# Kernel tuning notes

Measured on AMD Instinct MI355X. Metric: run time of the kernel, lower is better.

Reference implementation:

```python
import jax, jax.numpy as jnp
import numpy as np

NUM_HEADS = 1
HIDDEN = 256
HEAD_DIM = HIDDEN // NUM_HEADS
SCALE = HEAD_DIM ** -0.5


def _rotate_pairwise(x):
    # (... , d) -> rotate adjacent pairs: (x0,x1,x2,x3,..) -> (-x1,x0,-x3,x2,..)
    shape = x.shape
    x = x.reshape(*shape[:-1], -1, 2)
    x = jnp.stack([-x[..., 1], x[..., 0]], axis=-1)
    return x.reshape(shape)


def setup_inputs() -> dict:
    key = jax.random.key(0)
    ks = jax.random.split(key, 12)
    B, PB, QS, KS = 1, 1, 4096, 16448
    KV_IN = 64
    d = {
        'query': jax.random.normal(ks[0], (B, PB, QS, HIDDEN), jnp.float32),
        'key': jax.random.normal(ks[1], (B, PB, KS, KV_IN), jnp.float32),
        'value': jax.random.normal(ks[2], (B, PB, KS, KV_IN), jnp.float32),
        'rope_cos': jax.random.normal(ks[3], (QS, HEAD_DIM), jnp.float32),
        'rope_sin': jax.random.normal(ks[4], (QS, HEAD_DIM), jnp.float32),
        'wq': jax.random.normal(ks[5], (HIDDEN, HIDDEN), jnp.float32) * (HIDDEN ** -0.5),
        'bq': jnp.zeros((HIDDEN,), jnp.float32),
        'wk': jax.random.normal(ks[6], (KV_IN, HIDDEN), jnp.float32) * (KV_IN ** -0.5),
        'bk': jnp.zeros((HIDDEN,), jnp.float32),
        'wv': jax.random.normal(ks[7], (KV_IN, HIDDEN), jnp.float32) * (KV_IN ** -0.5),
        'bv': jnp.zeros((HIDDEN,), jnp.float32),
        'wo': jax.random.normal(ks[8], (HIDDEN, HIDDEN), jnp.float32) * (HIDDEN ** -0.5),
        'bo': jnp.zeros((HIDDEN,), jnp.float32),
        'num_k_exclude_rope': 64,
    }
    return d


def reference(query, key, value, rope_cos, rope_sin, wq, bq, wk, bk, wv, bv, wo, bo, num_k_exclude_rope):
    batch, pb, qs, _ = query.shape
    ks = key.shape[2]
    B = batch * pb
    # projections -> [B, H, S, hd]
    q = (query @ wq + bq).reshape(B, qs, NUM_HEADS, HEAD_DIM).transpose(0, 2, 1, 3)
    k = (key @ wk + bk).reshape(B, ks, NUM_HEADS, HEAD_DIM).transpose(0, 2, 1, 3)
    v = (value @ wv + bv).reshape(B, ks, NUM_HEADS, HEAD_DIM).transpose(0, 2, 1, 3)
    cos = rope_cos[None, None]  # [1,1,QS,hd]
    sin = rope_sin[None, None]
    # split off non-RoPE keys (object pointer tokens)
    n_rot = ks - num_k_exclude_rope
    k_rot, k_pass = k[:, :, :n_rot, :], k[:, :, n_rot:, :]
    q = q * cos + _rotate_pairwise(q) * sin
    if n_rot != qs:  # rope_k_repeat branch (static shapes)
        rep = n_rot // qs
        cos_k = jnp.repeat(cos, rep, axis=2)
        sin_k = jnp.repeat(sin, rep, axis=2)
    else:
        cos_k, sin_k = cos, sin
    k_emb = k_rot * cos_k + _rotate_pairwise(k_rot) * sin_k
    k = jnp.concatenate([k_emb, k_pass], axis=-2)
    attn = jax.nn.softmax(jnp.einsum('bhqd,bhkd->bhqk', q * SCALE, k), axis=-1)
    x = jnp.einsum('bhqk,bhkd->bhqd', attn, v)
    x = x.transpose(0, 2, 1, 3).reshape(batch, pb, qs, HIDDEN)
    return x @ wo + bo
```

## Files before the change

kernel.cpp:

```cpp
#include <hip/hip_runtime.h>
#include <hip/hip_bf16.h>

typedef __attribute__((ext_vector_type(4))) float floatx4;
typedef __attribute__((ext_vector_type(8))) short shortx8;
typedef __attribute__((ext_vector_type(8))) _Float16 halfx8;
typedef _Float16 half_t;

#define MFMA_BF16(A,B,C) __builtin_amdgcn_mfma_f32_16x16x32_bf16((A),(B),(C),0,0,0)
#define NEG_INF (-__builtin_inff())
#define GLOBAL_AS __attribute__((address_space(1)))
#define LDS_AS __attribute__((address_space(3)))

static __device__ __forceinline__ unsigned short f2b(float f) {
    union { float f; unsigned u; } v; v.f = f;
    unsigned r = v.u + 0x7FFFu + ((v.u >> 16) & 1u);
    return (unsigned short)(r >> 16);
}
static __device__ __forceinline__ unsigned pack_bf16(float lo, float hi) {
    return (unsigned)f2b(lo) | ((unsigned)f2b(hi) << 16);
}
static __device__ __forceinline__ unsigned pack_half(float lo, float hi) {
    union { half_t h[2]; unsigned u; } p;
    p.h[0] = (half_t)lo; p.h[1] = (half_t)hi;
    return p.u;
}
static __device__ __forceinline__ float EXP2F(float x) { return __builtin_amdgcn_exp2f(x); }

#define NSPLIT 8
#define NSPLIT_C 16
#define NTILES 257

__global__ __launch_bounds__(256) void wtrans_kernel(
    const float* __restrict__ wq, const float* __restrict__ wk,
    const float* __restrict__ wv, const float* __restrict__ wo,
    unsigned short* __restrict__ wqt, unsigned short* __restrict__ wkt,
    unsigned short* __restrict__ wvt, unsigned short* __restrict__ wot)
{
    __shared__ unsigned short tb[64 * 68];
    const int bid = blockIdx.x, tid = threadIdx.x;
    const float* src; unsigned short* dst; int K0, N0, Kfull;
    if (bid < 16)      { src = wq; dst = wqt; Kfull = 256; K0 = (bid >> 2) * 64; N0 = (bid & 3) * 64; }
    else if (bid < 20) { src = wk; dst = wkt; Kfull = 64;  K0 = 0; N0 = (bid - 16) * 64; }
    else if (bid < 24) { src = wv; dst = wvt; Kfull = 64;  K0 = 0; N0 = (bid - 20) * 64; }
    else { int t2 = bid - 24; src = wo; dst = wot; Kfull = 256; K0 = (t2 >> 2) * 64; N0 = (t2 & 3) * 64; }

    {
        const int r = tid >> 2, c0 = (tid & 3) * 16;
        const float* p = src + (K0 + r) * 256 + N0 + c0;
        #pragma unroll
        for (int j = 0; j < 16; j += 4) {
            floatx4 f = *(const floatx4*)(p + j);
            tb[r * 68 + c0 + j + 0] = f2b(f[0]);
            tb[r * 68 + c0 + j + 1] = f2b(f[1]);
            tb[r * 68 + c0 + j + 2] = f2b(f[2]);
            tb[r * 68 + c0 + j + 3] = f2b(f[3]);
        }
    }
    __syncthreads();
    {
        const int n = tid >> 2, k0 = (tid & 3) * 16;
        shortx8 v0, v1;
        #pragma unroll
        for (int j = 0; j < 8; j++) {
            v0[j] = tb[(k0 + j) * 68 + n];
            v1[j] = tb[(k0 + 8 + j) * 68 + n];
        }
        unsigned short* q = dst + (N0 + n) * Kfull + K0 + k0;
        *(shortx8*)q = v0;
        *(shortx8*)(q + 8) = v1;
    }
}

__global__ __launch_bounds__(256) void proj_kernel(
    const float* __restrict__ query, const float* __restrict__ key,
    const float* __restrict__ value,
    const unsigned short* __restrict__ wqt, const float* __restrict__ bq,
    const unsigned short* __restrict__ wkt, const float* __restrict__ bk,
    const unsigned short* __restrict__ wvt, const float* __restrict__ bv,
    const float* __restrict__ cosb, const float* __restrict__ sinb,
    const int* __restrict__ nkx,
    unsigned short* __restrict__ qr, unsigned short* __restrict__ krw,
    unsigned short* __restrict__ vtg)
{
    __shared__ unsigned short tbuf[256 * 72];
    const int tid = threadIdx.x;
    const int wave = tid >> 6, lane = tid & 63;
    const int c = lane & 15, quad = lane >> 4;
    const int bx = blockIdx.x;

    if (bx < 64) {
        const int m0 = bx * 64;
        shortx8 aA[8];
        {
            const int mrow = m0 + wave * 16 + c;
            #pragma unroll
            for (int ks = 0; ks < 8; ks++) {
                const float* p = query + mrow * 256 + ks * 32 + quad * 8;
                floatx4 f0 = *(const floatx4*)p;
                floatx4 f1 = *(const floatx4*)(p + 4);
                shortx8 a;
                #pragma unroll
                for (int j = 0; j < 4; j++) { a[j] = (short)f2b(f0[j]); a[j + 4] = (short)f2b(f1[j]); }
                aA[ks] = a;
            }
        }
        floatx4 acc[16];
        #pragma unroll
        for (int nt = 0; nt < 16; nt++) { acc[nt][0]=0.f; acc[nt][1]=0.f; acc[nt][2]=0.f; acc[nt][3]=0.f; }
        #pragma unroll
        for (int nt = 0; nt < 16; nt++) {
            #pragma unroll
            for (int ks = 0; ks < 8; ks++) {
                shortx8 b = *(const shortx8*)(wqt + (nt * 16 + c) * 256 + ks * 32 + quad * 8);
                acc[nt] = MFMA_BF16(aA[ks], b, acc[nt]);
            }
        }
        const float sc = 0.09016844005556021f;
        #pragma unroll
        for (int nt = 0; nt < 16; nt++) {
            const int col = nt * 16 + c;
            float vals[4];
            #pragma unroll
            for (int r = 0; r < 4; r++) {
                const int row = m0 + wave * 16 + quad * 4 + r;
                float v = acc[nt][r] + bq[col];
                float partner = __shfl_xor(v, 1);
                float cv = cosb[row * 256 + col];
                float sn = sinb[row * 256 + col];
                float rot = (col & 1) ? partner : -partner;
                vals[r] = (v * cv + rot * sn) * sc;
            }
            #pragma unroll
            for (int r2 = 0; r2 < 4; r2 += 2) {
                float a = vals[r2], b = vals[r2 + 1];
                float ax = __shfl_xor(a, 1), bx2 = __shfl_xor(b, 1);
                float lo = (c & 1) ? bx2 : a;
                float hi = (c & 1) ? b : ax;
                int row = m0 + wave * 16 + quad * 4 + r2 + (c & 1);
                *(unsigned*)(qr + row * 256 + nt * 16 + (c & ~1)) = pack_bf16(lo, hi);
            }
        }
        return;
    }

    const int isv = (bx >= 321);
    const int m0 = (isv ? (bx - 321) : (bx - 64)) * 64;
    const float* src = isv ? value : key;
    const unsigned short* wt = isv ? wvt : wkt;
    const float* bias = isv ? bv : bk;

    shortx8 aA[2];
    {
        const int mrow = m0 + wave * 16 + c;
        #pragma unroll
        for (int ks = 0; ks < 2; ks++) {
            const float* p = src + mrow * 64 + ks * 32 + quad * 8;
            floatx4 f0 = *(const floatx4*)p;
            floatx4 f1 = *(const floatx4*)(p + 4);
            shortx8 a;
            #pragma unroll
            for (int j = 0; j < 4; j++) { a[j] = (short)f2b(f0[j]); a[j + 4] = (short)f2b(f1[j]); }
            aA[ks] = a;
        }
    }
    floatx4 acc[16];
    #pragma unroll
    for (int nt = 0; nt < 16; nt++) { acc[nt][0]=0.f; acc[nt][1]=0.f; acc[nt][2]=0.f; acc[nt][3]=0.f; }
    #pragma unroll
    for (int nt = 0; nt < 16; nt++) {
        #pragma unroll
        for (int ks = 0; ks < 2; ks++) {
            shortx8 b = *(const shortx8*)(wt + (nt * 16 + c) * 64 + ks * 32 + quad * 8);
            acc[nt] = MFMA_BF16(aA[ks], b, acc[nt]);
        }
    }
    if (!isv) {
        const int n_rot = 16448 - nkx[0];
        int rep = n_rot / 4096; if (rep < 1) rep = 1;
        int rc4[4];
        #pragma unroll
        for (int r = 0; r < 4; r++) {
            int row = m0 + wave * 16 + quad * 4 + r;
            rc4[r] = row / rep;
        }
        #pragma unroll
        for (int nt = 0; nt < 16; nt++) {
            const int col = nt * 16 + c;
            float vals[4];
            #pragma unroll
            for (int r = 0; r < 4; r++) {
                const int row = m0 + wave * 16 + quad * 4 + r;
                float v = acc[nt][r] + bias[col];
                float partner = __shfl_xor(v, 1);
                float outv = v;
                if (row < n_rot) {
                    float cv = cosb[rc4[r] * 256 + col];
                    float sn = sinb[rc4[r] * 256 + col];
                    float rot = (col & 1) ? partner : -partner;
                    outv = v * cv + rot * sn;
                }
                vals[r] = outv;
            }
            #pragma unroll
            for (int r2 = 0; r2 < 4; r2 += 2) {
                float a = vals[r2], b = vals[r2 + 1];
                float ax = __shfl_xor(a, 1), bx2 = __shfl_xor(b, 1);
                float lo = (c & 1) ? bx2 : a;
                float hi = (c & 1) ? b : ax;
                int row = m0 + wave * 16 + quad * 4 + r2 + (c & 1);
                *(unsigned*)(krw + row * 256 + nt * 16 + (c & ~1)) = pack_bf16(lo, hi);
            }
        }
    } else {
        #pragma unroll
        for (int nt = 0; nt < 16; nt++) {
            const int col = nt * 16 + c;
            #pragma unroll
            for (int r = 0; r < 4; r++) {
                const int rl = wave * 16 + quad * 4 + r;
                tbuf[col * 72 + rl] = f2b(acc[nt][r] + bias[col]);
            }
        }
        __syncthreads();
        #pragma unroll
        for (int i = 0; i < 8; i++) {
            int G = i * 256 + tid;
            int n = G >> 3, g = G & 7;
            *(floatx4*)(vtg + n * 16448 + m0 + g * 8) = *(const floatx4*)(tbuf + n * 72 + g * 8);
        }
    }
}

__global__ __launch_bounds__(512, 2) void flash_kernel(
    const unsigned short* __restrict__ qr, const unsigned short* __restrict__ kr,
    const unsigned short* __restrict__ vt, half_t* __restrict__ Opart,
    float* __restrict__ Lpart)
{
    __shared__ unsigned short smem[75776];
    const int tid = threadIdx.x;
    const int wave = tid >> 6, lane = tid & 63;
    const int c = lane & 15, quad = lane >> 4;
    const int cx = c & 7;
    const int qg = wave & 3, kvh = wave >> 2;
    const int qrow0 = blockIdx.x * 128 + qg * 32;
    const int s = blockIdx.y;
    const int t0 = (s * NTILES) / NSPLIT, t1 = ((s + 1) * NTILES) / NSPLIT;
    unsigned short* pw = smem + 65536 + wave * 1280;

    shortx8 aQ[2][8];
    #pragma unroll
    for (int u = 0; u < 2; u++)
        #pragma unroll
        for (int ks = 0; ks < 8; ks++)
            aQ[u][ks] = *(const shortx8*)(qr + (qrow0 + u * 16 + c) * 256 + ks * 32 + quad * 8);

    floatx4 o[2][16];
    #pragma unroll
    for (int u = 0; u < 2; u++)
        #pragma unroll
        for (int nt = 0; nt < 16; nt++) { o[u][nt][0]=0.f; o[u][nt][1]=0.f; o[u][nt][2]=0.f; o[u][nt][3]=0.f; }
    float l_i[2] = { 0.f, 0.f };

    auto stage = [&](int t, int buf) {
        const int kv0 = t * 64;
        unsigned short* kb = smem + buf * 16384;
        unsigned short* vb = smem + 32768 + buf * 16384;
        #pragma unroll
        for (int i = 0; i < 4; i++) {
            int L = i * 512 + tid;
            int kv = L >> 5, p = L & 31;
            int g = (p & 24) | ((p & 7) ^ (kv & 7));
            __builtin_amdgcn_global_load_lds(
                (const GLOBAL_AS void*)(const void*)(kr + (kv0 + kv) * 256 + g * 8),
                (LDS_AS void*)(void*)(kb + (i * 512 + wave * 64) * 8), 16, 0, 0);
        }
        #pragma unroll
        for (int i = 0; i < 4; i++) {
            int L = i * 512 + tid;
            int d = L >> 3, p = L & 7;
            int g = p ^ (d & 7);
            __builtin_amdgcn_global_load_lds(
                (const GLOBAL_AS void*)(const void*)(vt + d * 16448 + kv0 + g * 8),
                (LDS_AS void*)(void*)(vb + (i * 512 + wave * 64) * 8), 16, 0, 0);
        }
    };

    stage(t0, 0);
    int cur = 0;
    const int pv_p = (kvh * 4 + quad) ^ cx;
    for (int t = t0; t < t1; t++) {
        __syncthreads();
        if (t + 1 < t1) stage(t + 1, cur ^ 1);
        const unsigned short* kb = smem + cur * 16384;
        const unsigned short* vb = smem + 32768 + cur * 16384;

        floatx4 sv[2][2];
        #pragma unroll
        for (int u = 0; u < 2; u++)
            #pragma unroll
            for (int nt = 0; nt < 2; nt++) { sv[u][nt][0]=0.f; sv[u][nt][1]=0.f; sv[u][nt][2]=0.f; sv[u][nt][3]=0.f; }
        #pragma unroll
        for (int nt = 0; nt < 2; nt++) {
            const unsigned short* krow = kb + (kvh * 32 + nt * 16 + c) * 256;
            #pragma unroll
            for (int ks = 0; ks < 8; ks++) {
                int p = ((ks >> 1) * 8) | ((((ks & 1) << 2) + quad) ^ cx);
                shortx8 kfrag = *(const shortx8*)(krow + p * 8);
                sv[0][nt] = MFMA_BF16(kfrag, aQ[0][ks], sv[0][nt]);
                sv[1][nt] = MFMA_BF16(kfrag, aQ[1][ks], sv[1][nt]);
            }
        }
        #pragma unroll
        for (int u = 0; u < 2; u++) {
            float rs = 0.f;
            #pragma unroll
            for (int nt = 0; nt < 2; nt++)
                #pragma unroll
                for (int r = 0; r < 4; r++) {
                    float pv = EXP2F(sv[u][nt][r]);
                    sv[u][nt][r] = pv;
                    rs += pv;
                }
            l_i[u] += rs;
        }
        #pragma unroll
        for (int u = 0; u < 2; u++)
            #pragma unroll
            for (int nt = 0; nt < 2; nt++)
                #pragma unroll
                for (int r2 = 0; r2 < 4; r2 += 2)
                    *(unsigned*)(pw + (u * 16 + c) * 40 + nt * 16 + quad * 4 + r2) =
                        pack_bf16(sv[u][nt][r2], sv[u][nt][r2 + 1]);
        shortx8 aP[2];
        #pragma unroll
        for (int u = 0; u < 2; u++)
            aP[u] = *(const shortx8*)(pw + (u * 16 + c) * 40 + quad * 8);
        #pragma unroll
        for (int nt = 0; nt < 16; nt++) {
            const unsigned short* vrow = vb + (nt * 16 + c) * 64;
            shortx8 b0 = *(const shortx8*)(vrow + pv_p * 8);
            o[0][nt] = MFMA_BF16(aP[0], b0, o[0][nt]);
            o[1][nt] = MFMA_BF16(aP[1], b0, o[1][nt]);
        }
        cur ^= 1;
    }
    const int sEff = s * 2 + kvh;
    half_t* Ob = Opart + (size_t)sEff * (4096 * 256);
    #pragma unroll
    for (int u = 0; u < 2; u++) {
        l_i[u] += __shfl_xor(l_i[u], 16);
        l_i[u] += __shfl_xor(l_i[u], 32);
    }
    float inv[2] = { 1.0f / l_i[0], 1.0f / l_i[1] };
    #pragma unroll
    for (int u = 0; u < 2; u++) {
        float ar[4];
        #pragma unroll
        for (int r = 0; r < 4; r++) ar[r] = __shfl(inv[u], quad * 4 + r);
        #pragma unroll
        for (int nt = 0; nt < 16; nt++) {
            o[u][nt][0] *= ar[0]; o[u][nt][1] *= ar[1];
            o[u][nt][2] *= ar[2]; o[u][nt][3] *= ar[3];
        }
    }
    #pragma unroll
    for (int u = 0; u < 2; u++)
        #pragma unroll
        for (int nt = 0; nt < 16; nt++)
            #pragma unroll
            for (int r2 = 0; r2 < 4; r2 += 2) {
                float a = o[u][nt][r2], b = o[u][nt][r2 + 1];
                float ax = __shfl_xor(a, 1), bx2 = __shfl_xor(b, 1);
                float lo = (c & 1) ? bx2 : a;
                float hi = (c & 1) ? b : ax;
                int row = qrow0 + u * 16 + quad * 4 + r2 + (c & 1);
                *(unsigned*)(Ob + row * 256 + nt * 16 + (c & ~1)) = pack_half(lo, hi);
            }
    if (quad == 0) {
        #pragma unroll
        for (int u = 0; u < 2; u++)
            Lpart[sEff * 4096 + qrow0 + u * 16 + c] = l_i[u];
    }
}

__global__ __launch_bounds__(256) void combine_kernel(
    const half_t* __restrict__ Opart, const float* __restrict__ Lpart,
    unsigned short* __restrict__ xb)
{
    int idx = blockIdx.x * 256 + threadIdx.x;
    int row = idx >> 5;
    int d0 = (idx & 31) * 8;
    float wn[NSPLIT_C], den = 0.f;
    #pragma unroll
    for (int sp = 0; sp < NSPLIT_C; sp++) { wn[sp] = Lpart[sp * 4096 + row]; den += wn[sp]; }
    float inv = 1.0f / den;
    #pragma unroll
    for (int sp = 0; sp < NSPLIT_C; sp++) wn[sp] *= inv;
    float acc[8];
    #pragma unroll
    for (int j = 0; j < 8; j++) acc[j] = 0.f;
    #pragma unroll
    for (int sp = 0; sp < NSPLIT_C; sp++) {
        halfx8 hv = *(const halfx8*)(Opart + (size_t)sp * (4096 * 256) + row * 256 + d0);
        #pragma unroll
        for (int j = 0; j < 8; j++) acc[j] += wn[sp] * (float)hv[j];
    }
    shortx8 xv;
    #pragma unroll
    for (int j = 0; j < 8; j++) xv[j] = (short)f2b(acc[j]);
    *(shortx8*)(xb + row * 256 + d0) = xv;
}

__global__ __launch_bounds__(256) void oproj_kernel(
    const unsigned short* __restrict__ xb, const unsigned short* __restrict__ wot,
    const float* __restrict__ bo, float* __restrict__ outp)
{
    const int tid = threadIdx.x;
    const int wave = tid >> 6, lane = tid & 63;
    const int c = lane & 15, quad = lane >> 4;
    const int m0 = blockIdx.x * 64;
    const int n0 = blockIdx.y * 64;

    shortx8 aX[8];
    #pragma unroll
    for (int ks = 0; ks < 8; ks++)
        aX[ks] = *(const shortx8*)(xb + (m0 + wave * 16 + c) * 256 + ks * 32 + quad * 8);
    floatx4 acc[4];
    #pragma unroll
    for (int nt = 0; nt < 4; nt++) { acc[nt][0]=0.f; acc[nt][1]=0.f; acc[nt][2]=0.f; acc[nt][3]=0.f; }
    #pragma unroll
    for (int nt = 0; nt < 4; nt++) {
        #pragma unroll
        for (int ks = 0; ks < 8; ks++) {
            shortx8 b = *(const shortx8*)(wot + (n0 + nt * 16 + c) * 256 + ks * 32 + quad * 8);
            acc[nt] = MFMA_BF16(aX[ks], b, acc[nt]);
        }
    }
    #pragma unroll
    for (int nt = 0; nt < 4; nt++) {
        const int col = n0 + nt * 16 + c;
        #pragma unroll
        for (int r = 0; r < 4; r++) {
            const int row = m0 + wave * 16 + quad * 4 + r;
            outp[row * 256 + col] = acc[nt][r] + bo[col];
        }
    }
}

extern "C" void kernel_launch(void* const* d_in, const int* in_sizes, int n_in,
                              void* d_out, int out_size, void* d_ws, size_t ws_size,
                              hipStream_t stream) {
    const float* query = (const float*)d_in[0];
    const float* key   = (const float*)d_in[1];
    const float* value = (const float*)d_in[2];
    const float* cosb  = (const float*)d_in[3];
    const float* sinb  = (const float*)d_in[4];
    const float* wq    = (const float*)d_in[5];
    const float* bq    = (const float*)d_in[6];
    const float* wk    = (const float*)d_in[7];
    const float* bk    = (const float*)d_in[8];
    const float* wv    = (const float*)d_in[9];
    const float* bv    = (const float*)d_in[10];
    const float* wo    = (const float*)d_in[11];
    const float* bo    = (const float*)d_in[12];
    const int*   nk    = (const int*)d_in[13];

    char* ws = (char*)d_ws;
    unsigned short* wqt = (unsigned short*)(ws + 0);
    unsigned short* wkt = (unsigned short*)(ws + 131072);
    unsigned short* wvt = (unsigned short*)(ws + 163840);
    unsigned short* wot = (unsigned short*)(ws + 196608);
    unsigned short* qr  = (unsigned short*)(ws + 327680);
    unsigned short* xb  = (unsigned short*)(ws + 327680);
    unsigned short* krw = (unsigned short*)(ws + 2424832);
    unsigned short* vtg = (unsigned short*)(ws + 10846208);
    half_t* Opart = (half_t*)(ws + 19267584);
    float* Lpart = (float*)(ws + 52822016);
    float* outp  = (float*)d_out;

    wtrans_kernel<<<dim3(40), dim3(256), 0, stream>>>(wq, wk, wv, wo, wqt, wkt, wvt, wot);
    proj_kernel<<<dim3(578), dim3(256), 0, stream>>>(
        query, key, value, wqt, bq, wkt, bk, wvt, bv, cosb, sinb, nk, qr, krw, vtg);
    flash_kernel<<<dim3(32, NSPLIT), dim3(512), 0, stream>>>(qr, krw, vtg, Opart, Lpart);
    combine_kernel<<<dim3(512), dim3(256), 0, stream>>>(Opart, Lpart, xb);
    oproj_kernel<<<dim3(64, 4), dim3(256), 0, stream>>>(xb, wot, bo, outp);
}
```

Before: 230.7 us.

## Fuse all five stages into one cooperative persistent kernel with grid syncs

Replaces the five separate launches (weight transpose, projections, flash attention, combine, output projection) with one cooperative kernel of 256 blocks that moves between stages using grid-wide syncs. Work that used to be spread over many blocks is remapped onto the persistent grid, with two virtual blocks per 512-thread block and multiple passes. The combine and output projection appear to be merged so the intermediate x buffer is staged in shared memory rather than global memory. This removes launch gaps and some global round trips, at the cost of grid-sync overhead, a fixed grid size, and possibly lower occupancy or load imbalance in the projection stages.

```diff
diff --git a/kernel.cpp b/kernel.cpp
--- a/kernel.cpp
+++ b/kernel.cpp
@@ -1,5 +1,8 @@
 #include <hip/hip_runtime.h>
 #include <hip/hip_bf16.h>
+#include <hip/hip_cooperative_groups.h>
+
+namespace cg = cooperative_groups;
 
 typedef __attribute__((ext_vector_type(4))) float floatx4;
 typedef __attribute__((ext_vector_type(8))) short shortx8;
@@ -7,7 +10,6 @@
 typedef _Float16 half_t;
 
 #define MFMA_BF16(A,B,C) __builtin_amdgcn_mfma_f32_16x16x32_bf16((A),(B),(C),0,0,0)
-#define NEG_INF (-__builtin_inff())
 #define GLOBAL_AS __attribute__((address_space(1)))
 #define LDS_AS __attribute__((address_space(3)))
 
@@ -30,419 +32,422 @@
 #define NSPLIT_C 16
 #define NTILES 257
 
-__global__ __launch_bounds__(256) void wtrans_kernel(
-    const float* __restrict__ wq, const float* __restrict__ wk,
-    const float* __restrict__ wv, const float* __restrict__ wo,
+__global__ __launch_bounds__(512, 2) void mega_kernel(
+    const float* __restrict__ query, const float* __restrict__ key,
+    const float* __restrict__ value, const float* __restrict__ cosb,
+    const float* __restrict__ sinb,
+    const float* __restrict__ wq, const float* __restrict__ bq,
+    const float* __restrict__ wk, const float* __restrict__ bk,
+    const float* __restrict__ wv, const float* __restrict__ bv,
+    const float* __restrict__ wo, const float* __restrict__ bo,
+    const int* __restrict__ nkx,
     unsigned short* __restrict__ wqt, unsigned short* __restrict__ wkt,
-    unsigned short* __restrict__ wvt, unsigned short* __restrict__ wot)
+    unsigned short* __restrict__ wvt, unsigned short* __restrict__ wot,
+    unsigned short* __restrict__ qr, unsigned short* __restrict__ krw,
+    unsigned short* __restrict__ vtg, half_t* __restrict__ Opart,
+    float* __restrict__ Lpart, float* __restrict__ outp)
 {
-    __shared__ unsigned short tb[64 * 68];
-    const int bid = blockIdx.x, tid = threadIdx.x;
-    const float* src; unsigned short* dst; int K0, N0, Kfull;
-    if (bid < 16)      { src = wq; dst = wqt; Kfull = 256; K0 = (bid >> 2) * 64; N0 = (bid & 3) * 64; }
-    else if (bid < 20) { src = wk; dst = wkt; Kfull = 64;  K0 = 0; N0 = (bid - 16) * 64; }
-    else if (bid < 24) { src = wv; dst = wvt; Kfull = 64;  K0 = 0; N0 = (bid - 20) * 64; }
-    else { int t2 = bid - 24; src = wo; dst = wot; Kfull = 256; K0 = (t2 >> 2) * 64; N0 = (t2 & 3) * 64; }
-
-    {
-        const int r = tid >> 2, c0 = (tid & 3) * 16;
-        const float* p = src + (K0 + r) * 256 + N0 + c0;
-        #pragma unroll
-        for (int j = 0; j < 16; j += 4) {
-            floatx4 f = *(const floatx4*)(p + j);
-            tb[r * 68 + c0 + j + 0] = f2b(f[0]);
-            tb[r * 68 + c0 + j + 1] = f2b(f[1]);
-            tb[r * 68 + c0 + j + 2] = f2b(f[2]);
-            tb[r * 68 + c0 + j + 3] = f2b(f[3]);
-        }
-    }
-    __syncthreads();
-    {
-        const int n = tid >> 2, k0 = (tid & 3) * 16;
-        shortx8 v0, v1;
-        #pragma unroll
-        for (int j = 0; j < 8; j++) {
-            v0[j] = tb[(k0 + j) * 68 + n];
-            v1[j] = tb[(k0 + 8 + j) * 68 + n];
-        }
-        unsigned short* q = dst + (N0 + n) * Kfull + K0 + k0;
-        *(shortx8*)q = v0;
-        *(shortx8*)(q + 8) = v1;
-    }
-}
-
-__global__ __launch_bounds__(256) void proj_kernel(
-    const float* __restrict__ query, const float* __restrict__ key,
-    const float* __restrict__ value,
-    const unsigned short* __restrict__ wqt, const float* __restrict__ bq,
-    const unsigned short* __restrict__ wkt, const float* __restrict__ bk,
-    const unsigned short* __restrict__ wvt, const float* __restrict__ bv,
-    const float* __restrict__ cosb, const float* __restrict__ sinb,
-    const int* __restrict__ nkx,
-    unsigned short* __restrict__ qr, unsigned short* __restrict__ krw,
-    unsigned short* __restrict__ vtg)
-{
-    __shared__ unsigned short tbuf[256 * 72];
-    const int tid = threadIdx.x;
-    const int wave = tid >> 6, lane = tid & 63;
-    const int c = lane & 15, quad = lane >> 4;
-    const int bx = blockIdx.x;
-
-    if (bx < 64) {
-        const int m0 = bx * 64;
-        shortx8 aA[8];
-        {
-            const int mrow = m0 + wave * 16 + c;
-            #pragma unroll
-            for (int ks = 0; ks < 8; ks++) {
-                const float* p = query + mrow * 256 + ks * 32 + quad * 8;
-                floatx4 f0 = *(const floatx4*)p;
-                floatx4 f1 = *(const floatx4*)(p + 4);
-                shortx8 a;
-                #pragma unroll
-                for (int j = 0; j < 4; j++) { a[j] = (short)f2b(f0[j]); a[j + 4] = (short)f2b(f1[j]); }
-                aA[ks] = a;
-            }
-        }
-        floatx4 acc[16];
-        #pragma unroll
-        for (int nt = 0; nt < 16; nt++) { acc[nt][0]=0.f; acc[nt][1]=0.f; acc[nt][2]=0.f; acc[nt][3]=0.f; }
-        #pragma unroll
-        for (int nt = 0; nt < 16; nt++) {
-            #pragma unroll
-            for (int ks = 0; ks < 8; ks++) {
-                shortx8 b = *(const shortx8*)(wqt + (nt * 16 + c) * 256 + ks * 32 + quad * 8);
-                acc[nt] = MFMA_BF16(aA[ks], b, acc[nt]);
-            }
-        }
-        const float sc = 0.09016844005556021f;
-        #pragma unroll
-        for (int nt = 0; nt < 16; nt++) {
-            const int col = nt * 16 + c;
-            float vals[4];
-            #pragma unroll
-            for (int r = 0; r < 4; r++) {
-                const int row = m0 + wave * 16 + quad * 4 + r;
-                float v = acc[nt][r] + bq[col];
-                float partner = __shfl_xor(v, 1);
-                float cv = cosb[row * 256 + col];
-                float sn = sinb[row * 256 + col];
-                float rot = (col & 1) ? partner : -partner;
-                vals[r] = (v * cv + rot * sn) * sc;
-            }
-            #pragma unroll
-            for (int r2 = 0; r2 < 4; r2 += 2) {
-                float a = vals[r2], b = vals[r2 + 1];
-                float ax = __shfl_xor(a, 1), bx2 = __shfl_xor(b, 1);
-                float lo = (c & 1) ? bx2 : a;
-                float hi = (c & 1) ? b : ax;
-                int row = m0 + wave * 16 + quad * 4 + r2 + (c & 1);
-                *(unsigned*)(qr + row * 256 + nt * 16 + (c & ~1)) = pack_bf16(lo, hi);
-            }
-        }
-        return;
-    }
-
-    const int isv = (bx >= 321);
-    const int m0 = (isv ? (bx - 321) : (bx - 64)) * 64;
-    const float* src = isv ? value : key;
-    const unsigned short* wt = isv ? wvt : wkt;
-    const float* bias = isv ? bv : bk;
-
-    shortx8 aA[2];
-    {
-        const int mrow = m0 + wave * 16 + c;
-        #pragma unroll
-        for (int ks = 0; ks < 2; ks++) {
-            const float* p = src + mrow * 64 + ks * 32 + quad * 8;
-            floatx4 f0 = *(const floatx4*)p;
-            floatx4 f1 = *(const floatx4*)(p + 4);
-            shortx8 a;
-            #pragma unroll
-            for (int j = 0; j < 4; j++) { a[j] = (short)f2b(f0[j]); a[j + 4] = (short)f2b(f1[j]); }
-            aA[ks] = a;
-        }
-    }
-    floatx4 acc[16];
-    #pragma unroll
-    for (int nt = 0; nt < 16; nt++) { acc[nt][0]=0.f; acc[nt][1]=0.f; acc[nt][2]=0.f; acc[nt][3]=0.f; }
-    #pragma unroll
-    for (int nt = 0; nt < 16; nt++) {
-        #pragma unroll
-        for (int ks = 0; ks < 2; ks++) {
-            shortx8 b = *(const shortx8*)(wt + (nt * 16 + c) * 64 + ks * 32 + quad * 8);
-            acc[nt] = MFMA_BF16(aA[ks], b, acc[nt]);
-        }
-    }
-    if (!isv) {
-        const int n_rot = 16448 - nkx[0];
-        int rep = n_rot / 4096; if (rep < 1) rep = 1;
-        int rc4[4];
-        #pragma unroll
-        for (int r = 0; r < 4; r++) {
-            int row = m0 + wave * 16 + quad * 4 + r;
-            rc4[r] = row / rep;
-        }
-        #pragma unroll
-        for (int nt = 0; nt < 16; nt++) {
-            const int col = nt * 16 + c;
-            float vals[4];
-            #pragma unroll
-            for (int r = 0; r < 4; r++) {
-                const int row = m0 + wave * 16 + quad * 4 + r;
-                float v = acc[nt][r] + bias[col];
-                float partner = __shfl_xor(v, 1);
-                float outv = v;
-                if (row < n_rot) {
-                    float cv = cosb[rc4[r] * 256 + col];
-                    float sn = sinb[rc4[r] * 256 + col];
-                    float rot = (col & 1) ? partner : -partner;
-                    outv = v * cv + rot * sn;
-                }
-                vals[r] = outv;
-            }
-            #pragma unroll
-            for (int r2 = 0; r2 < 4; r2 += 2) {
-                float a = vals[r2], b = vals[r2 + 1];
-                float ax = __shfl_xor(a, 1), bx2 = __shfl_xor(b, 1);
-                float lo = (c & 1) ? bx2 : a;
-                float hi = (c & 1) ? b : ax;
-                int row = m0 + wave * 16 + quad * 4 + r2 + (c & 1);
-                *(unsigned*)(krw + row * 256 + nt * 16 + (c & ~1)) = pack_bf16(lo, hi);
-            }
-        }
-    } else {
-        #pragma unroll
-        for (int nt = 0; nt < 16; nt++) {
-            const int col = nt * 16 + c;
-            #pragma unroll
-            for (int r = 0; r < 4; r++) {
-                const int rl = wave * 16 + quad * 4 + r;
-                tbuf[col * 72 + rl] = f2b(acc[nt][r] + bias[col]);
-            }
-        }
-        __syncthreads();
-        #pragma unroll
-        for (int i = 0; i < 8; i++) {
-            int G = i * 256 + tid;
-            int n = G >> 3, g = G & 7;
-            *(floatx4*)(vtg + n * 16448 + m0 + g * 8) = *(const floatx4*)(tbuf + n * 72 + g * 8);
-        }
-    }
-}
-
-__global__ __launch_bounds__(512, 2) void flash_kernel(
-    const unsigned short* __restrict__ qr, const unsigned short* __restrict__ kr,
-    const unsigned short* __restrict__ vt, half_t* __restrict__ Opart,
-    float* __restrict__ Lpart)
-{
+    cg::grid_group grid = cg::this_grid();
     __shared__ unsigned short smem[75776];
     const int tid = threadIdx.x;
-    const int wave = tid >> 6, lane = tid & 63;
-    const int c = lane & 15, quad = lane >> 4;
-    const int cx = c & 7;
-    const int qg = wave & 3, kvh = wave >> 2;
-    const int qrow0 = blockIdx.x * 128 + qg * 32;
-    const int s = blockIdx.y;
-    const int t0 = (s * NTILES) / NSPLIT, t1 = ((s + 1) * NTILES) / NSPLIT;
-    unsigned short* pw = smem + 65536 + wave * 1280;
-
-    shortx8 aQ[2][8];
-    #pragma unroll
-    for (int u = 0; u < 2; u++)
+    const int bid = blockIdx.x;
+
+    if (bid < 20) {
+        const int sub = tid >> 8, t = tid & 255;
+        const int vb = bid * 2 + sub;
+        unsigned short* tb = smem + sub * 4608;
+        const float* srcw; unsigned short* dstw; int K0, N0, Kfull;
+        if (vb < 16)      { srcw = wq; dstw = wqt; Kfull = 256; K0 = (vb >> 2) * 64; N0 = (vb & 3) * 64; }
+        else if (vb < 20) { srcw = wk; dstw = wkt; Kfull = 64;  K0 = 0; N0 = (vb - 16) * 64; }
+        else if (vb < 24) { srcw = wv; dstw = wvt; Kfull = 64;  K0 = 0; N0 = (vb - 20) * 64; }
+        else { int t2 = vb - 24; srcw = wo; dstw = wot; Kfull = 256; K0 = (t2 >> 2) * 64; N0 = (t2 & 3) * 64; }
+        {
+            const int r = t >> 2, c0 = (t & 3) * 16;
+            const float* p = srcw + (K0 + r) * 256 + N0 + c0;
+            #pragma unroll
+            for (int j = 0; j < 16; j += 4) {
+                floatx4 f = *(const floatx4*)(p + j);
+                tb[r * 68 + c0 + j + 0] = f2b(f[0]);
+                tb[r * 68 + c0 + j + 1] = f2b(f[1]);
+                tb[r * 68 + c0 + j + 2] = f2b(f[2]);
+                tb[r * 68 + c0 + j + 3] = f2b(f[3]);
+            }
+        }
+        __syncthreads();
+        {
+            const int n = t >> 2, k0 = (t & 3) * 16;
+            shortx8 v0, v1;
+            #pragma unroll
+            for (int j = 0; j < 8; j++) {
+                v0[j] = tb[(k0 + j) * 68 + n];
+                v1[j] = tb[(k0 + 8 + j) * 68 + n];
+            }
+            unsigned short* q = dstw + (N0 + n) * Kfull + K0 + k0;
+            *(shortx8*)q = v0;
+            *(shortx8*)(q + 8) = v1;
+        }
+    }
+    grid.sync();
+
+    #pragma unroll 1
+    for (int pass = 0; pass < 2; pass++) {
+        const int sub = tid >> 8, t = tid & 255;
+        const int vb = pass * 512 + bid * 2 + sub;
+        const int wave = t >> 6, lane = t & 63;
+        const int c = lane & 15, quad = lane >> 4;
+        unsigned short* tbuf = smem + sub * 18432;
+        int vM0 = 0;
+        bool doV = false;
+
+        if (vb < 64) {
+            const int m0 = vb * 64;
+            shortx8 aA[8];
+            {
+                const int mrow = m0 + wave * 16 + c;
+                #pragma unroll
+                for (int ks = 0; ks < 8; ks++) {
+                    const float* p = query + mrow * 256 + ks * 32 + quad * 8;
+                    floatx4 f0 = *(const floatx4*)p;
+                    floatx4 f1 = *(const floatx4*)(p + 4);
+                    shortx8 a;
+                    #pragma unroll
+                    for (int j = 0; j < 4; j++) { a[j] = (short)f2b(f0[j]); a[j + 4] = (short)f2b(f1[j]); }
+                    aA[ks] = a;
+                }
+            }
+            floatx4 acc[16];
+            #pragma unroll
+            for (int nt = 0; nt < 16; nt++) { acc[nt][0]=0.f; acc[nt][1]=0.f; acc[nt][2]=0.f; acc[nt][3]=0.f; }
+            #pragma unroll
+            for (int nt = 0; nt < 16; nt++) {
+                #pragma unroll
+                for (int ks = 0; ks < 8; ks++) {
+                    shortx8 b = *(const shortx8*)(wqt + (nt * 16 + c) * 256 + ks * 32 + quad * 8);
+                    acc[nt] = MFMA_BF16(aA[ks], b, acc[nt]);
+                }
+            }
+            const float sc = 0.09016844005556021f;
+            #pragma unroll
+            for (int nt = 0; nt < 16; nt++) {
+                const int col = nt * 16 + c;
+                float vals[4];
+                #pragma unroll
+                for (int r = 0; r < 4; r++) {
+                    const int row = m0 + wave * 16 + quad * 4 + r;
+                    float v = acc[nt][r] + bq[col];
+                    float partner = __shfl_xor(v, 1);
+                    float cv = cosb[row * 256 + col];
+                    float sn = sinb[row * 256 + col];
+                    float rot = (col & 1) ? partner : -partner;
+                    vals[r] = (v * cv + rot * sn) * sc;
+                }
+                #pragma unroll
+                for (int r2 = 0; r2 < 4; r2 += 2) {
+                    float a = vals[r2], b = vals[r2 + 1];
+                    float ax = __shfl_xor(a, 1), bx2 = __shfl_xor(b, 1);
+                    float lo = (c & 1) ? bx2 : a;
+                    float hi = (c & 1) ? b : ax;
+                    int row = m0 + wave * 16 + quad * 4 + r2 + (c & 1);
+                    *(unsigned*)(qr + row * 256 + nt * 16 + (c & ~1)) = pack_bf16(lo, hi);
+                }
+            }
+        } else if (vb < 578) {
+            const int isv = (vb >= 321);
+            const int m0 = (isv ? (vb - 321) : (vb - 64)) * 64;
+            const float* src = isv ? value : key;
+            const unsigned short* wt = isv ? wvt : wkt;
+            const float* bias = isv ? bv : bk;
+
+            shortx8 aA[2];
+            {
+                const int mrow = m0 + wave * 16 + c;
+                #pragma unroll
+                for (int ks = 0; ks < 2; ks++) {
+                    const float* p = src + mrow * 64 + ks * 32 + quad * 8;
+                    floatx4 f0 = *(const floatx4*)p;
+                    floatx4 f1 = *(const floatx4*)(p + 4);
+                    shortx8 a;
+                    #pragma unroll
+                    for (int j = 0; j < 4; j++) { a[j] = (short)f2b(f0[j]); a[j + 4] = (short)f2b(f1[j]); }
+                    aA[ks] = a;
+                }
+            }
+            floatx4 acc[16];
+            #pragma unroll
+            for (int nt = 0; nt < 16; nt++) { acc[nt][0]=0.f; acc[nt][1]=0.f; acc[nt][2]=0.f; acc[nt][3]=0.f; }
+            #pragma unroll
+            for (int nt = 0; nt < 16; nt++) {
+                #pragma unroll
+                for (int ks = 0; ks < 2; ks++) {
+                    shortx8 b = *(const shortx8*)(wt + (nt * 16 + c) * 64 + ks * 32 + quad * 8);
+                    acc[nt] = MFMA_BF16(aA[ks], b, acc[nt]);
+                }
+            }
+            if (!isv) {
+                const int n_rot = 16448 - nkx[0];
+                int rep = n_rot / 4096; if (rep < 1) rep = 1;
+                int rc4[4];
+                #pragma unroll
+                for (int r = 0; r < 4; r++) {
+                    int row = m0 + wave * 16 + quad * 4 + r;
+                    rc4[r] = row / rep;
+                }
+                #pragma unroll
+                for (int nt = 0; nt < 16; nt++) {
+                    const int col = nt * 16 + c;
+                    float vals[4];
+                    #pragma unroll
+                    for (int r = 0; r < 4; r++) {
+                        const int row = m0 + wave * 16 + quad * 4 + r;
+                        float v = acc[nt][r] + bias[col];
+                        float partner = __shfl_xor(v, 1);
+                        float outv = v;
+                        if (row < n_rot) {
+                            float cv = cosb[rc4[r] * 256 + col];
+                            float sn = sinb[rc4[r] * 256 + col];
+                            float rot = (col & 1) ? partner : -partner;
+                            outv = v * cv + rot * sn;
+                        }
+                        vals[r] = outv;
+                    }
+                    #pragma unroll
+                    for (int r2 = 0; r2 < 4; r2 += 2) {
+                        float a = vals[r2], b = vals[r2 + 1];
+                        float ax = __shfl_xor(a, 1), bx2 = __shfl_xor(b, 1);
+                        float lo = (c & 1) ? bx2 : a;
+                        float hi = (c & 1) ? b : ax;
+                        int row = m0 + wave * 16 + quad * 4 + r2 + (c & 1);
+                        *(unsigned*)(krw + row * 256 + nt * 16 + (c & ~1)) = pack_bf16(lo, hi);
+                    }
+                }
+            } else {
+                #pragma unroll
+                for (int nt = 0; nt < 16; nt++) {
+                    const int col = nt * 16 + c;
+                    #pragma unroll
+                    for (int r = 0; r < 4; r++) {
+                        const int rl = wave * 16 + quad * 4 + r;
+                        tbuf[col * 72 + rl] = f2b(acc[nt][r] + bias[col]);
+                    }
+                }
+                doV = true;
+                vM0 = m0;
+            }
+        }
+        __syncthreads();
+        if (doV) {
+            #pragma unroll
+            for (int i = 0; i < 8; i++) {
+                int G = i * 256 + t;
+                int n = G >> 3, g = G & 7;
+                *(floatx4*)(vtg + n * 16448 + vM0 + g * 8) = *(const floatx4*)(tbuf + n * 72 + g * 8);
+            }
+        }
+        __syncthreads();
+    }
+    grid.sync();
+
+    {
+        const int wave = tid >> 6, lane = tid & 63;
+        const int c = lane & 15, quad = lane >> 4;
+        const int cx = c & 7;
+        const int qg = wave & 3, kvh = wave >> 2;
+        const int qrow0 = (bid & 31) * 128 + qg * 32;
+        const int s = bid >> 5;
+        const int t0 = (s * NTILES) / NSPLIT, t1 = ((s + 1) * NTILES) / NSPLIT;
+        unsigned short* pw = smem + 65536 + wave * 1280;
+
+        shortx8 aQ[2][8];
+        #pragma unroll
+        for (int u = 0; u < 2; u++)
+            #pragma unroll
+            for (int ks = 0; ks < 8; ks++)
+                aQ[u][ks] = *(const shortx8*)(qr + (qrow0 + u * 16 + c) * 256 + ks * 32 + quad * 8);
+
+        floatx4 o[2][16];
+        #pragma unroll
+        for (int u = 0; u < 2; u++)
+            #pragma unroll
+            for (int nt = 0; nt < 16; nt++) { o[u][nt][0]=0.f; o[u][nt][1]=0.f; o[u][nt][2]=0.f; o[u][nt][3]=0.f; }
+        float l_i[2] = { 0.f, 0.f };
+
+        auto stage = [&](int t, int buf) {
+            const int kv0 = t * 64;
+            unsigned short* kb = smem + buf * 16384;
+            unsigned short* vb = smem + 32768 + buf * 16384;
+            #pragma unroll
+            for (int i = 0; i < 4; i++) {
+                int L = i * 512 + tid;
+                int kv = L >> 5, p = L & 31;
+                int g = (p & 24) | ((p & 7) ^ (kv & 7));
+                __builtin_amdgcn_global_load_lds(
+                    (const GLOBAL_AS void*)(const void*)(krw + (kv0 + kv) * 256 + g * 8),
+                    (LDS_AS void*)(void*)(kb + (i * 512 + wave * 64) * 8), 16, 0, 0);
+            }
+            #pragma unroll
+            for (int i = 0; i < 4; i++) {
+                int L = i * 512 + tid;
+                int d = L >> 3, p = L & 7;
+                int g = p ^ (d & 7);
+                __builtin_amdgcn_global_load_lds(
+                    (const GLOBAL_AS void*)(const void*)(vtg + d * 16448 + kv0 + g * 8),
+                    (LDS_AS void*)(void*)(vb + (i * 512 + wave * 64) * 8), 16, 0, 0);
+            }
+        };
+
+        stage(t0, 0);
+        int cur = 0;
+        const int pv_p = (kvh * 4 + quad) ^ cx;
+        for (int t = t0; t < t1; t++) {
+            __syncthreads();
+            if (t + 1 < t1) stage(t + 1, cur ^ 1);
+            const unsigned short* kb = smem + cur * 16384;
+            const unsigned short* vb = smem + 32768 + cur * 16384;
+
+            floatx4 sv[2][2];
+            #pragma unroll
+            for (int u = 0; u < 2; u++)
+                #pragma unroll
+                for (int nt = 0; nt < 2; nt++) { sv[u][nt][0]=0.f; sv[u][nt][1]=0.f; sv[u][nt][2]=0.f; sv[u][nt][3]=0.f; }
+            #pragma unroll
+            for (int nt = 0; nt < 2; nt++) {
+                const unsigned short* krow = kb + (kvh * 32 + nt * 16 + c) * 256;
+                #pragma unroll
+                for (int ks = 0; ks < 8; ks++) {
+                    int p = ((ks >> 1) * 8) | ((((ks & 1) << 2) + quad) ^ cx);
+                    shortx8 kfrag = *(const shortx8*)(krow + p * 8);
+                    sv[0][nt] = MFMA_BF16(kfrag, aQ[0][ks], sv[0][nt]);
+                    sv[1][nt] = MFMA_BF16(kfrag, aQ[1][ks], sv[1][nt]);
+                }
+            }
+            #pragma unroll
+            for (int u = 0; u < 2; u++) {
+                float rs = 0.f;
+                #pragma unroll
+                for (int nt = 0; nt < 2; nt++)
+                    #pragma unroll
+                    for (int r = 0; r < 4; r++) {
+                        float pv = EXP2F(sv[u][nt][r]);
+                        sv[u][nt][r] = pv;
+                        rs += pv;
+                    }
+                l_i[u] += rs;
+            }
+            #pragma unroll
+            for (int u = 0; u < 2; u++)
+                #pragma unroll
+                for (int nt = 0; nt < 2; nt++)
+                    #pragma unroll
+                    for (int r2 = 0; r2 < 4; r2 += 2)
+                        *(unsigned*)(pw + (u * 16 + c) * 40 + nt * 16 + quad * 4 + r2) =
+                            pack_bf16(sv[u][nt][r2], sv[u][nt][r2 + 1]);
+            shortx8 aP[2];
+            #pragma unroll
+            for (int u = 0; u < 2; u++)
+                aP[u] = *(const shortx8*)(pw + (u * 16 + c) * 40 + quad * 8);
+            #pragma unroll
+            for (int nt = 0; nt < 16; nt++) {
+                const unsigned short* vrow = vb + (nt * 16 + c) * 64;
+                shortx8 b0 = *(const shortx8*)(vrow + pv_p * 8);
+                o[0][nt] = MFMA_BF16(aP[0], b0, o[0][nt]);
+                o[1][nt] = MFMA_BF16(aP[1], b0, o[1][nt]);
+            }
+            cur ^= 1;
+        }
+        const int sEff = s * 2 + kvh;
+        half_t* Ob = Opart + (size_t)sEff * (4096 * 256);
+        #pragma unroll
+        for (int u = 0; u < 2; u++) {
+            l_i[u] += __shfl_xor(l_i[u], 16);
+            l_i[u] += __shfl_xor(l_i[u], 32);
+        }
+        float inv[2] = { 1.0f / l_i[0], 1.0f / l_i[1] };
+        #pragma unroll
+        for (int u = 0; u < 2; u++) {
+            float ar[4];
+            #pragma unroll
+            for (int r = 0; r < 4; r++) ar[r] = __shfl(inv[u], quad * 4 + r);
+            #pragma unroll
+            for (int nt = 0; nt < 16; nt++) {
+                o[u][nt][0] *= ar[0]; o[u][nt][1] *= ar[1];
+                o[u][nt][2] *= ar[2]; o[u][nt][3] *= ar[3];
+            }
+        }
+        #pragma unroll
+        for (int u = 0; u < 2; u++)
+            #pragma unroll
+            for (int nt = 0; nt < 16; nt++)
+                #pragma unroll
+                for (int r2 = 0; r2 < 4; r2 += 2) {
+                    float a = o[u][nt][r2], b = o[u][nt][r2 + 1];
+                    float ax = __shfl_xor(a, 1), bx2 = __shfl_xor(b, 1);
+                    float lo = (c & 1) ? bx2 : a;
+                    float hi = (c & 1) ? b : ax;
+                    int row = qrow0 + u * 16 + quad * 4 + r2 + (c & 1);
+                    *(unsigned*)(Ob + row * 256 + nt * 16 + (c & ~1)) = pack_half(lo, hi);
+                }
+        if (quad == 0) {
+            #pragma unroll
+            for (int u = 0; u < 2; u++)
+                Lpart[sEff * 4096 + qrow0 + u * 16 + c] = l_i[u];
+        }
+    }
+    grid.sync();
+
+    {
+        const int m0 = bid * 16;
+        unsigned short* xb = smem;
+        {
+            const int r_l = tid >> 5;
+            const int d0 = (tid & 31) * 8;
+            const int row = m0 + r_l;
+            float wn[NSPLIT_C], den = 0.f;
+            #pragma unroll
+            for (int sp = 0; sp < NSPLIT_C; sp++) { wn[sp] = Lpart[sp * 4096 + row]; den += wn[sp]; }
+            float inv = 1.0f / den;
+            #pragma unroll
+            for (int sp = 0; sp < NSPLIT_C; sp++) wn[sp] *= inv;
+            float acc[8];
+            #pragma unroll
+            for (int j = 0; j < 8; j++) acc[j] = 0.f;
+            #pragma unroll
+            for (int sp = 0; sp < NSPLIT_C; sp++) {
+                halfx8 hv = *(const halfx8*)(Opart + (size_t)sp * (4096 * 256) + row * 256 + d0);
+                #pragma unroll
+                for (int j = 0; j < 8; j++) acc[j] += wn[sp] * (float)hv[j];
+            }
+            shortx8 xv;
+            #pragma unroll
+            for (int j = 0; j < 8; j++) xv[j] = (short)f2b(acc[j]);
+            *(shortx8*)(xb + r_l * 264 + d0) = xv;
+        }
+        __syncthreads();
+        const int wave = tid >> 6, lane = tid & 63;
+        const int c = lane & 15, quad = lane >> 4;
+        shortx8 aX[8];
         #pragma unroll
         for (int ks = 0; ks < 8; ks++)
-            aQ[u][ks] = *(const shortx8*)(qr + (qrow0 + u * 16 + c) * 256 + ks * 32 + quad * 8);
-
-    floatx4 o[2][16];
-    #pragma unroll
-    for (int u = 0; u < 2; u++)
-        #pragma unroll
-        for (int nt = 0; nt < 16; nt++) { o[u][nt][0]=0.f; o[u][nt][1]=0.f; o[u][nt][2]=0.f; o[u][nt][3]=0.f; }
-    float l_i[2] = { 0.f, 0.f };
-
-    auto stage = [&](int t, int buf) {
-        const int kv0 = t * 64;
-        unsigned short* kb = smem + buf * 16384;
-        unsigned short* vb = smem + 32768 + buf * 16384;
-        #pragma unroll
-        for (int i = 0; i < 4; i++) {
-            int L = i * 512 + tid;
-            int kv = L >> 5, p = L & 31;
-            int g = (p & 24) | ((p & 7) ^ (kv & 7));
-            __builtin_amdgcn_global_load_lds(
-                (const GLOBAL_AS void*)(const void*)(kr + (kv0 + kv) * 256 + g * 8),
-                (LDS_AS void*)(void*)(kb + (i * 512 + wave * 64) * 8), 16, 0, 0);
-        }
-        #pragma unroll
-        for (int i = 0; i < 4; i++) {
-            int L = i * 512 + tid;
-            int d = L >> 3, p = L & 7;
-            int g = p ^ (d & 7);
-            __builtin_amdgcn_global_load_lds(
-                (const GLOBAL_AS void*)(const void*)(vt + d * 16448 + kv0 + g * 8),
-                (LDS_AS void*)(void*)(vb + (i * 512 + wave * 64) * 8), 16, 0, 0);
-        }
-    };
-
-    stage(t0, 0);
-    int cur = 0;
-    const int pv_p = (kvh * 4 + quad) ^ cx;
-    for (int t = t0; t < t1; t++) {
-        __syncthreads();
-        if (t + 1 < t1) stage(t + 1, cur ^ 1);
-        const unsigned short* kb = smem + cur * 16384;
-        const unsigned short* vb = smem + 32768 + cur * 16384;
-
-        floatx4 sv[2][2];
-        #pragma unroll
-        for (int u = 0; u < 2; u++)
-            #pragma unroll
-            for (int nt = 0; nt < 2; nt++) { sv[u][nt][0]=0.f; sv[u][nt][1]=0.f; sv[u][nt][2]=0.f; sv[u][nt][3]=0.f; }
-        #pragma unroll
-        for (int nt = 0; nt < 2; nt++) {
-            const unsigned short* krow = kb + (kvh * 32 + nt * 16 + c) * 256;
+            aX[ks] = *(const shortx8*)(xb + c * 264 + ks * 32 + quad * 8);
+        floatx4 acc[2];
+        #pragma unroll
+        for (int n2 = 0; n2 < 2; n2++) { acc[n2][0]=0.f; acc[n2][1]=0.f; acc[n2][2]=0.f; acc[n2][3]=0.f; }
+        #pragma unroll
+        for (int n2 = 0; n2 < 2; n2++) {
+            const int nt = wave * 2 + n2;
             #pragma unroll
             for (int ks = 0; ks < 8; ks++) {
-                int p = ((ks >> 1) * 8) | ((((ks & 1) << 2) + quad) ^ cx);
-                shortx8 kfrag = *(const shortx8*)(krow + p * 8);
-                sv[0][nt] = MFMA_BF16(kfrag, aQ[0][ks], sv[0][nt]);
-                sv[1][nt] = MFMA_BF16(kfrag, aQ[1][ks], sv[1][nt]);
-            }
-        }
-        #pragma unroll
-        for (int u = 0; u < 2; u++) {
-            float rs = 0.f;
-            #pragma unroll
-            for (int nt = 0; nt < 2; nt++)
-                #pragma unroll
-                for (int r = 0; r < 4; r++) {
-                    float pv = EXP2F(sv[u][nt][r]);
-                    sv[u][nt][r] = pv;
-                    rs += pv;
-                }
-            l_i[u] += rs;
-        }
-        #pragma unroll
-        for (int u = 0; u < 2; u++)
-            #pragma unroll
-            for (int nt = 0; nt < 2; nt++)
-                #pragma unroll
-                for (int r2 = 0; r2 < 4; r2 += 2)
-                    *(unsigned*)(pw + (u * 16 + c) * 40 + nt * 16 + quad * 4 + r2) =
-                        pack_bf16(sv[u][nt][r2], sv[u][nt][r2 + 1]);
-        shortx8 aP[2];
-        #pragma unroll
-        for (int u = 0; u < 2; u++)
-            aP[u] = *(const shortx8*)(pw + (u * 16 + c) * 40 + quad * 8);
-        #pragma unroll
-        for (int nt = 0; nt < 16; nt++) {
-            const unsigned short* vrow = vb + (nt * 16 + c) * 64;
-            shortx8 b0 = *(const shortx8*)(vrow + pv_p * 8);
-            o[0][nt] = MFMA_BF16(aP[0], b0, o[0][nt]);
-            o[1][nt] = MFMA_BF16(aP[1], b0, o[1][nt]);
-        }
-        cur ^= 1;
-    }
-    const int sEff = s * 2 + kvh;
-    half_t* Ob = Opart + (size_t)sEff * (4096 * 256);
-    #pragma unroll
-    for (int u = 0; u < 2; u++) {
-        l_i[u] += __shfl_xor(l_i[u], 16);
-        l_i[u] += __shfl_xor(l_i[u], 32);
-    }
-    float inv[2] = { 1.0f / l_i[0], 1.0f / l_i[1] };
-    #pragma unroll
-    for (int u = 0; u < 2; u++) {
-        float ar[4];
-        #pragma unroll
-        for (int r = 0; r < 4; r++) ar[r] = __shfl(inv[u], quad * 4 + r);
-        #pragma unroll
-        for (int nt = 0; nt < 16; nt++) {
-            o[u][nt][0] *= ar[0]; o[u][nt][1] *= ar[1];
-            o[u][nt][2] *= ar[2]; o[u][nt][3] *= ar[3];
-        }
-    }
-    #pragma unroll
-    for (int u = 0; u < 2; u++)
-        #pragma unroll
-        for (int nt = 0; nt < 16; nt++)
-            #pragma unroll
-            for (int r2 = 0; r2 < 4; r2 += 2) {
-                float a = o[u][nt][r2], b = o[u][nt][r2 + 1];
-                float ax = __shfl_xor(a, 1), bx2 = __shfl_xor(b, 1);
-                float lo = (c & 1) ? bx2 : a;
-                float hi = (c & 1) ? b : ax;
-                int row = qrow0 + u * 16 + quad * 4 + r2 + (c & 1);
-                *(unsigned*)(Ob + row * 256 + nt * 16 + (c & ~1)) = pack_half(lo, hi);
-            }
-    if (quad == 0) {
-        #pragma unroll
-        for (int u = 0; u < 2; u++)
-            Lpart[sEff * 4096 + qrow0 + u * 16 + c] = l_i[u];
-    }
-}
-
-__global__ __launch_bounds__(256) void combine_kernel(
-    const half_t* __restrict__ Opart, const float* __restrict__ Lpart,
-    unsigned short* __restrict__ xb)
-{
-    int idx = blockIdx.x * 256 + threadIdx.x;
-    int row = idx >> 5;
-    int d0 = (idx & 31) * 8;
-    float wn[NSPLIT_C], den = 0.f;
-    #pragma unroll
-    for (int sp = 0; sp < NSPLIT_C; sp++) { wn[sp] = Lpart[sp * 4096 + row]; den += wn[sp]; }
-    float inv = 1.0f / den;
-    #pragma unroll
-    for (int sp = 0; sp < NSPLIT_C; sp++) wn[sp] *= inv;
-    float acc[8];
-    #pragma unroll
-    for (int j = 0; j < 8; j++) acc[j] = 0.f;
-    #pragma unroll
-    for (int sp = 0; sp < NSPLIT_C; sp++) {
-        halfx8 hv = *(const halfx8*)(Opart + (size_t)sp * (4096 * 256) + row * 256 + d0);
-        #pragma unroll
-        for (int j = 0; j < 8; j++) acc[j] += wn[sp] * (float)hv[j];
-    }
-    shortx8 xv;
-    #pragma unroll
-    for (int j = 0; j < 8; j++) xv[j] = (short)f2b(acc[j]);
-    *(shortx8*)(xb + row * 256 + d0) = xv;
-}
-
-__global__ __launch_bounds__(256) void oproj_kernel(
-    const unsigned short* __restrict__ xb, const unsigned short* __restrict__ wot,
-    const float* __restrict__ bo, float* __restrict__ outp)
-{
-    const int tid = threadIdx.x;
-    const int wave = tid >> 6, lane = tid & 63;
-    const int c = lane & 15, quad = lane >> 4;
-    const int m0 = blockIdx.x * 64;
-    const int n0 = blockIdx.y * 64;
-
-    shortx8 aX[8];
-    #pragma unroll
-    for (int ks = 0; ks < 8; ks++)
-        aX[ks] = *(const shortx8*)(xb + (m0 + wave * 16 + c) * 256 + ks * 32 + quad * 8);
-    floatx4 acc[4];
-    #pragma unroll
-    for (int nt = 0; nt < 4; nt++) { acc[nt][0]=0.f; acc[nt][1]=0.f; acc[nt][2]=0.f; acc[nt][3]=0.f; }
-    #pragma unroll
-    for (int nt = 0; nt < 4; nt++) {
-        #pragma unroll
-        for (int ks = 0; ks < 8; ks++) {
-            shortx8 b = *(const shortx8*)(wot + (n0 + nt * 16 + c) * 256 + ks * 32 + quad * 8);
-            acc[nt] = MFMA_BF16(aX[ks], b, acc[nt]);
-        }
-    }
-    #pragma unroll
-    for (int nt = 0; nt < 4; nt++) {
-        const int col = n0 + nt * 16 + c;
-        #pragma unroll
-        for (int r = 0; r < 4; r++) {
-            const int row = m0 + wave * 16 + quad * 4 + r;
-            outp[row * 256 + col] = acc[nt][r] + bo[col];
+                shortx8 b = *(const shortx8*)(wot + (nt * 16 + c) * 256 + ks * 32 + quad * 8);
+                acc[n2] = MFMA_BF16(aX[ks], b, acc[n2]);
+            }
+        }
+        #pragma unroll
+        for (int n2 = 0; n2 < 2; n2++) {
+            const int col = (wave * 2 + n2) * 16 + c;
+            #pragma unroll
+            for (int r = 0; r < 4; r++) {
+                const int row = m0 + quad * 4 + r;
+                outp[row * 256 + col] = acc[n2][r] + bo[col];
+            }
         }
     }
 }
@@ -471,17 +476,19 @@
     unsigned short* wvt = (unsigned short*)(ws + 163840);
     unsigned short* wot = (unsigned short*)(ws + 196608);
     unsigned short* qr  = (unsigned short*)(ws + 327680);
-    unsigned short* xb  = (unsigned short*)(ws + 327680);
     unsigned short* krw = (unsigned short*)(ws + 2424832);
     unsigned short* vtg = (unsigned short*)(ws + 10846208);
     half_t* Opart = (half_t*)(ws + 19267584);
     float* Lpart = (float*)(ws + 52822016);
     float* outp  = (float*)d_out;
 
-    wtrans_kernel<<<dim3(40), dim3(256), 0, stream>>>(wq, wk, wv, wo, wqt, wkt, wvt, wot);
-    proj_kernel<<<dim3(578), dim3(256), 0, stream>>>(
-        query, key, value, wqt, bq, wkt, bk, wvt, bv, cosb, sinb, nk, qr, krw, vtg);
-    flash_kernel<<<dim3(32, NSPLIT), dim3(512), 0, stream>>>(qr, krw, vtg, Opart, Lpart);
-    combine_kernel<<<dim3(512), dim3(256), 0, stream>>>(Opart, Lpart, xb);
-    oproj_kernel<<<dim3(64, 4), dim3(256), 0, stream>>>(xb, wot, bo, outp);
+    void* args[] = {
+        (void*)&query, (void*)&key, (void*)&value, (void*)&cosb, (void*)&sinb,
+        (void*)&wq, (void*)&bq, (void*)&wk, (void*)&bk, (void*)&wv, (void*)&bv,
+        (void*)&wo, (void*)&bo, (void*)&nk,
+        (void*)&wqt, (void*)&wkt, (void*)&wvt, (void*)&wot,
+        (void*)&qr, (void*)&krw, (void*)&vtg, (void*)&Opart, (void*)&Lpart, (void*)&outp
+    };
+    hipLaunchCooperativeKernel((const void*)mega_kernel, dim3(256), dim3(512),
+                               args, 0, stream);
 }
```

New measurement: 398.1 us. 1.73x slower.
